# Performance work log

Hardware: AMD Instinct MI355X
Metric: run time of the kernel (lower is better)

Reference implementation:

```python
import jax, jax.numpy as jnp
import numpy as np

N = 262144   # total atoms (rows of x)
B = 512      # systems (segments)
E = 16       # experts
I = 256      # in_features
O_MOE = 128  # moe out channels (fraction_moe=0.5 of 256)
O_REG = 128  # regular Linear out channels


def setup_inputs() -> dict:
    key = jax.random.key(0)
    ks = jax.random.split(key, 6)
    k = 1.0 / np.sqrt(I)
    x = jax.random.normal(ks[0], (N, I), dtype=jnp.float32)
    coeff = jax.random.uniform(ks[1], (B, E), dtype=jnp.float32)
    routing_idxs = jnp.full((B,), N // B, dtype=jnp.int64)  # uniform segment lengths
    moe_weights = k * 2.0 * (jax.random.uniform(ks[2], (E, O_MOE, I), dtype=jnp.float32) - 0.5)
    moe_bias = k * 2.0 * (jax.random.uniform(ks[3], (O_MOE,), dtype=jnp.float32) - 0.5)
    lin_weight = k * 2.0 * (jax.random.uniform(ks[4], (O_REG, I), dtype=jnp.float32) - 0.5)
    lin_bias = k * 2.0 * (jax.random.uniform(ks[5], (O_REG,), dtype=jnp.float32) - 0.5)
    return {"x": x, "expert_mixing_coefficients": coeff, "routing_idxs": routing_idxs,
            "moe_weights": moe_weights, "moe_bias": moe_bias,
            "lin_weight": lin_weight, "lin_bias": lin_bias}


def reference(x, expert_mixing_coefficients, routing_idxs, moe_weights, moe_bias, lin_weight, lin_bias):
    b = expert_mixing_coefficients.shape[0]
    n, i = x.shape
    l = n // b  # uniform segment length (segment_mm with equal routing_idxs)
    # per-system mixed expert weights: [B, I, O_moe]
    w_mixed = jnp.einsum('eoi,be->bio', moe_weights, expert_mixing_coefficients)
    # grouped segment matmul: rows of segment b multiply w_mixed[b]
    moe_out = jnp.einsum('bli,bio->blo', x.reshape(b, l, i), w_mixed).reshape(n, -1) + moe_bias
    regular_out = x @ lin_weight.T + lin_bias
    return jnp.concatenate([moe_out, regular_out], axis=-1)
```

## Files before the change

kernel.cpp:

```cpp
#include <hip/hip_runtime.h>


#define NSEG   512
#define NEXP   16
#define KDIM   256
#define OMOE   128
#define OTOT   256
#define LSEG   512

typedef __attribute__((ext_vector_type(4))) float  f32x4;
typedef __attribute__((ext_vector_type(8))) short  bf16x8;
typedef __attribute__((ext_vector_type(4))) unsigned short u16x4;
typedef __attribute__((ext_vector_type(4))) unsigned int   u32x4;

__device__ __forceinline__ unsigned short bf16_rne(float v) {
  unsigned u = __builtin_bit_cast(unsigned, v);
  unsigned r = u + 0x7FFFu + ((u >> 16) & 1u);
  return (unsigned short)(r >> 16);
}
__device__ __forceinline__ void split2(float v, unsigned short& h, unsigned short& l) {
  h = bf16_rne(v);
  float hf = __builtin_bit_cast(float, ((unsigned)h) << 16);
  l = bf16_rne(v - hf);
}
__device__ __forceinline__ unsigned cvtpk(float a, float b) {
  unsigned r;
  asm("v_cvt_pk_bf16_f32 %0, %1, %2" : "=v"(r) : "v"(a), "v"(b));
  return r;
}
__device__ __forceinline__ void split8(f32x4 v0, f32x4 v1, bf16x8& h, bf16x8& l) {
  float a[8] = {v0[0], v0[1], v0[2], v0[3], v1[0], v1[1], v1[2], v1[3]};
  unsigned hw[4], lw[4];
  #pragma unroll
  for (int i = 0; i < 4; ++i) {
    unsigned hp = cvtpk(a[2 * i], a[2 * i + 1]);
    float hf0 = __builtin_bit_cast(float, hp << 16);
    float hf1 = __builtin_bit_cast(float, hp & 0xFFFF0000u);
    lw[i] = cvtpk(a[2 * i] - hf0, a[2 * i + 1] - hf1);
    hw[i] = hp;
  }
  u32x4 H = {hw[0], hw[1], hw[2], hw[3]};
  u32x4 L = {lw[0], lw[1], lw[2], lw[3]};
  h = __builtin_bit_cast(bf16x8, H);
  l = __builtin_bit_cast(bf16x8, L);
}


__global__ __launch_bounds__(256) void prep_moe_kernel(
    const float* __restrict__ moe_w, const float* __restrict__ coeff,
    unsigned short* __restrict__ wm) {
  __shared__ float wlds[NEXP][4][KDIM];
  const int t  = threadIdx.x;
  const int ot = blockIdx.x & 31;
  const int bc = blockIdx.x >> 5;
  const float* src = moe_w + (size_t)ot * 4 * KDIM;
  #pragma unroll
  for (int it = 0; it < 16; ++it) {
    int idx = it * 256 + t;
    int e = idx >> 8, rem = idx & 255;
    int o = rem >> 6, k4 = rem & 63;
    *(f32x4*)(&wlds[e][o][k4 * 4]) =
        *(const f32x4*)(src + (size_t)e * OMOE * KDIM + o * KDIM + k4 * 4);
  }
  __syncthreads();
  const int o = t >> 6, k4 = t & 63;
  const int og = ot * 4 + o;
  const int kt = k4 >> 3, ks = (k4 >> 1) & 3, jo = (k4 & 1) * 4;
  const int p  = og * 4 + (ks ^ ((og >> 1) & 3));
  const size_t woff = (size_t)kt * 8192 + p * 8 + jo;
  for (int bb = 0; bb < 32; ++bb) {
    const int b = bc * 32 + bb;
    const float* cf = coeff + (size_t)b * NEXP;
    f32x4 acc = (f32x4){0.f, 0.f, 0.f, 0.f};
    #pragma unroll
    for (int e = 0; e < NEXP; ++e) {
      const float c = cf[e];
      const f32x4 w = *(const f32x4*)(&wlds[e][o][k4 * 4]);
      #pragma unroll
      for (int j = 0; j < 4; ++j) acc[j] += c * w[j];
    }
    u16x4 hv, lv;
    #pragma unroll
    for (int j = 0; j < 4; ++j) {
      unsigned short h, l;
      split2(acc[j], h, l);
      hv[j] = h; lv[j] = l;
    }
    unsigned short* dst = wm + (size_t)b * 65536 + woff;
    *(u16x4*)(dst)        = hv;
    *(u16x4*)(dst + 4096) = lv;
  }
}

__global__ __launch_bounds__(256) void prep_lin_kernel(
    const float* __restrict__ lw, unsigned short* __restrict__ wl) {
  const int idx = blockIdx.x * 256 + threadIdx.x;
  const int o = idx >> 6, k4 = idx & 63;
  f32x4 v = *(const f32x4*)(lw + (size_t)idx * 4);
  const int kt = k4 >> 3, ks = (k4 >> 1) & 3, jo = (k4 & 1) * 4;
  const int p  = o * 4 + (ks ^ ((o >> 1) & 3));
  u16x4 hv, lv;
  #pragma unroll
  for (int j = 0; j < 4; ++j) {
    unsigned short h, l;
    split2(v[j], h, l);
    hv[j] = h; lv[j] = l;
  }
  unsigned short* dst = wl + (size_t)kt * 8192 + p * 8 + jo;
  *(u16x4*)(dst)        = hv;
  *(u16x4*)(dst + 4096) = lv;
}

#define GLOAD16(g, l) __builtin_amdgcn_global_load_lds(                      \
    (const __attribute__((address_space(1))) unsigned int*)(g),              \
    (__attribute__((address_space(3))) unsigned int*)(l), 16, 0, 0)

__global__ __launch_bounds__(512, 4) void gemm_kernel(
    const float* __restrict__ x,
    const unsigned short* __restrict__ wm, const unsigned short* __restrict__ wl,
    const float* __restrict__ moe_b, const float* __restrict__ lin_b,
    float* __restrict__ out) {
  __shared__ unsigned short lds[32768];
  const int t = threadIdx.x;
  const int wave = t >> 6, lane = t & 63;
  const int wrm = wave >> 1, wn = wave & 1;

  const int blk = blockIdx.x;
  const int wg = ((blk & 7) << 8) | (blk >> 3);
  const int b = wg >> 2, rt = wg & 3;
  const int row0 = b * LSEG + rt * 128;

  f32x4 acc[2][8] = {};

  const float* xbase = x + (size_t)(row0 + wrm * 32 + (lane & 15)) * KDIM + (lane >> 4) * 8;

  const int colb = wn * 128 + (lane & 15);
  const int ks = lane >> 4;
  const int boff0 = (colb * 4 + (ks ^ ((colb >> 1) & 3))) * 8;

  const unsigned short* wmb = wm + (size_t)b * 65536;

  auto stage_B = [&](int buf, int kt) {
    unsigned short* Bb = &lds[buf * 16384];
    const unsigned short* srcm = wmb + (size_t)kt * 8192;
    const unsigned short* srcl = wl  + (size_t)kt * 8192;
    #pragma unroll
    for (int part = 0; part < 2; ++part) {
      #pragma unroll
      for (int cc = 0; cc < 2; ++cc) {
        const int c = wave * 2 + cc;
        const unsigned short* src = (c < 8)
            ? (srcm + (size_t)part * 4096 + (c * 64 + lane) * 8)
            : (srcl + (size_t)part * 4096 + ((c - 8) * 64 + lane) * 8);
        GLOAD16(src, Bb + part * 8192 + c * 512);
      }
    }
  };

  bf16x8 ah[2], al[2];

  auto compute = [&](int buf) {
    const short* Bb = (const short*)&lds[buf * 16384];
    #pragma unroll
    for (int nt = 0; nt < 8; ++nt) {
      bf16x8 bh = *(const bf16x8*)(Bb + boff0 + nt * 512);
      bf16x8 bl = *(const bf16x8*)(Bb + 8192 + boff0 + nt * 512);
      #pragma unroll
      for (int mt = 0; mt < 2; ++mt) {
        acc[mt][nt] = __builtin_amdgcn_mfma_f32_16x16x32_bf16(ah[mt], bh, acc[mt][nt], 0, 0, 0);
        acc[mt][nt] = __builtin_amdgcn_mfma_f32_16x16x32_bf16(ah[mt], bl, acc[mt][nt], 0, 0, 0);
        acc[mt][nt] = __builtin_amdgcn_mfma_f32_16x16x32_bf16(al[mt], bh, acc[mt][nt], 0, 0, 0);
      }
    }
  };

  stage_B(0, 0);
  {
    const float* p0 = xbase;
    const float* p1 = xbase + 16 * KDIM;
    split8(*(const f32x4*)p0, *(const f32x4*)(p0 + 4), ah[0], al[0]);
    split8(*(const f32x4*)p1, *(const f32x4*)(p1 + 4), ah[1], al[1]);
  }
  __syncthreads();

  int buf = 0;
  for (int kt = 0; kt < 8; ++kt) {
    const bool pf = (kt < 7);
    f32x4 n0, n1, n2, n3;
    if (pf) {
      const float* p0 = xbase + (kt + 1) * 32;
      const float* p1 = p0 + 16 * KDIM;
      n0 = *(const f32x4*)p0; n1 = *(const f32x4*)(p0 + 4);
      n2 = *(const f32x4*)p1; n3 = *(const f32x4*)(p1 + 4);
      stage_B(buf ^ 1, kt + 1);
    }
    compute(buf);
    if (pf) {
      split8(n0, n1, ah[0], al[0]);
      split8(n2, n3, ah[1], al[1]);
    }
    __syncthreads();
    buf ^= 1;
  }

  #pragma unroll
  for (int nt = 0; nt < 8; ++nt) {
    const int col = wn * 128 + nt * 16 + (lane & 15);
    const float bias = (col < OMOE) ? moe_b[col] : lin_b[col - OMOE];
    #pragma unroll
    for (int mt = 0; mt < 2; ++mt) {
      const int rbase = row0 + wrm * 32 + mt * 16 + (lane >> 4) * 4;
      #pragma unroll
      for (int j = 0; j < 4; ++j)
        out[(size_t)(rbase + j) * OTOT + col] = acc[mt][nt][j] + bias;
    }
  }
}

extern "C" void kernel_launch(void* const* d_in, const int* in_sizes, int n_in,
                              void* d_out, int out_size, void* d_ws, size_t ws_size,
                              hipStream_t stream) {
  const float* x     = (const float*)d_in[0];
  const float* coeff = (const float*)d_in[1];
  const float* moe_w = (const float*)d_in[3];
  const float* moe_b = (const float*)d_in[4];
  const float* lin_w = (const float*)d_in[5];
  const float* lin_b = (const float*)d_in[6];
  float* out = (float*)d_out;

  unsigned short* wm = (unsigned short*)d_ws;
  unsigned short* wl = wm + (size_t)NSEG * 65536;

  prep_moe_kernel<<<dim3(512), dim3(256), 0, stream>>>(moe_w, coeff, wm);
  prep_lin_kernel<<<dim3(32), dim3(256), 0, stream>>>(lin_w, wl);
  gemm_kernel<<<dim3(2048), dim3(512), 0, stream>>>(x, wm, wl, moe_b, lin_b, out);
}
```

Baseline: 517.0 us.

## Split B staging into half-tile units with a deeper four-slot LDS ring

```diff
diff --git a/kernel.cpp b/kernel.cpp
--- a/kernel.cpp
+++ b/kernel.cpp
@@ -115,6 +115,8 @@
     (const __attribute__((address_space(1))) unsigned int*)(g),              \
     (__attribute__((address_space(3))) unsigned int*)(l), 16, 0, 0)
 
+#define MFMA(a, b, c) __builtin_amdgcn_mfma_f32_16x16x32_bf16((a), (b), (c), 0, 0, 0)
+
 __global__ __launch_bounds__(512, 4) void gemm_kernel(
     const float* __restrict__ x,
     const unsigned short* __restrict__ wm, const unsigned short* __restrict__ wl,
@@ -140,68 +142,84 @@
 
   const unsigned short* wmb = wm + (size_t)b * 65536;
 
-  auto stage_B = [&](int buf, int kt) {
-    unsigned short* Bb = &lds[buf * 16384];
-    const unsigned short* srcm = wmb + (size_t)kt * 8192;
-    const unsigned short* srcl = wl  + (size_t)kt * 8192;
-    #pragma unroll
-    for (int part = 0; part < 2; ++part) {
-      #pragma unroll
-      for (int cc = 0; cc < 2; ++cc) {
-        const int c = wave * 2 + cc;
-        const unsigned short* src = (c < 8)
-            ? (srcm + (size_t)part * 4096 + (c * 64 + lane) * 8)
-            : (srcl + (size_t)part * 4096 + ((c - 8) * 64 + lane) * 8);
-        GLOAD16(src, Bb + part * 8192 + c * 512);
-      }
+  auto stage_unit = [&](int u) {
+    const int kt = u >> 1, part = u & 1;
+    unsigned short* U = &lds[(u & 3) * 8192];
+    #pragma unroll
+    for (int cc = 0; cc < 2; ++cc) {
+      const int c = wave * 2 + cc;
+      const unsigned short* src = (c < 8)
+          ? (wmb + (size_t)kt * 8192 + part * 4096 + (c * 64 + lane) * 8)
+          : (wl  + (size_t)kt * 8192 + part * 4096 + ((c - 8) * 64 + lane) * 8);
+      GLOAD16(src, U + c * 512);
     }
   };
 
   bf16x8 ah[2], al[2];
 
-  auto compute = [&](int buf) {
-    const short* Bb = (const short*)&lds[buf * 16384];
+  auto compute_p0 = [&](int u) {
+    const short* U = (const short*)&lds[(u & 3) * 8192];
+    __builtin_amdgcn_s_setprio(1);
     #pragma unroll
     for (int nt = 0; nt < 8; ++nt) {
-      bf16x8 bh = *(const bf16x8*)(Bb + boff0 + nt * 512);
-      bf16x8 bl = *(const bf16x8*)(Bb + 8192 + boff0 + nt * 512);
-      #pragma unroll
-      for (int mt = 0; mt < 2; ++mt) {
-        acc[mt][nt] = __builtin_amdgcn_mfma_f32_16x16x32_bf16(ah[mt], bh, acc[mt][nt], 0, 0, 0);
-        acc[mt][nt] = __builtin_amdgcn_mfma_f32_16x16x32_bf16(ah[mt], bl, acc[mt][nt], 0, 0, 0);
-        acc[mt][nt] = __builtin_amdgcn_mfma_f32_16x16x32_bf16(al[mt], bh, acc[mt][nt], 0, 0, 0);
-      }
-    }
+      bf16x8 bh = *(const bf16x8*)(U + boff0 + nt * 512);
+      acc[0][nt] = MFMA(ah[0], bh, acc[0][nt]);
+      acc[1][nt] = MFMA(ah[1], bh, acc[1][nt]);
+      acc[0][nt] = MFMA(al[0], bh, acc[0][nt]);
+      acc[1][nt] = MFMA(al[1], bh, acc[1][nt]);
+    }
+    __builtin_amdgcn_s_setprio(0);
   };
-
-  stage_B(0, 0);
+  auto compute_p1 = [&](int u) {
+    const short* U = (const short*)&lds[(u & 3) * 8192];
+    __builtin_amdgcn_s_setprio(1);
+    #pragma unroll
+    for (int nt = 0; nt < 8; ++nt) {
+      bf16x8 bl = *(const bf16x8*)(U + boff0 + nt * 512);
+      acc[0][nt] = MFMA(ah[0], bl, acc[0][nt]);
+      acc[1][nt] = MFMA(ah[1], bl, acc[1][nt]);
+    }
+    __builtin_amdgcn_s_setprio(0);
+  };
+
+  stage_unit(0); stage_unit(1); stage_unit(2);
+  __builtin_amdgcn_sched_barrier(0);
   {
     const float* p0 = xbase;
     const float* p1 = xbase + 16 * KDIM;
     split8(*(const f32x4*)p0, *(const f32x4*)(p0 + 4), ah[0], al[0]);
     split8(*(const f32x4*)p1, *(const f32x4*)(p1 + 4), ah[1], al[1]);
   }
-  __syncthreads();
-
-  int buf = 0;
-  for (int kt = 0; kt < 8; ++kt) {
-    const bool pf = (kt < 7);
+  __builtin_amdgcn_s_barrier();
+  __builtin_amdgcn_sched_barrier(0);
+
+  for (int kt = 0; kt < 7; ++kt) {
+    const int u0 = kt * 2, u1 = u0 + 1;
+    stage_unit(u0 + 3);
+    __builtin_amdgcn_sched_barrier(0);
     f32x4 n0, n1, n2, n3;
-    if (pf) {
+    {
       const float* p0 = xbase + (kt + 1) * 32;
       const float* p1 = p0 + 16 * KDIM;
       n0 = *(const f32x4*)p0; n1 = *(const f32x4*)(p0 + 4);
       n2 = *(const f32x4*)p1; n3 = *(const f32x4*)(p1 + 4);
-      stage_B(buf ^ 1, kt + 1);
-    }
-    compute(buf);
-    if (pf) {
-      split8(n0, n1, ah[0], al[0]);
-      split8(n2, n3, ah[1], al[1]);
-    }
-    __syncthreads();
-    buf ^= 1;
-  }
+    }
+    compute_p0(u0);
+    __builtin_amdgcn_s_barrier();
+    __builtin_amdgcn_sched_barrier(0);
+    if (kt < 6) stage_unit(u1 + 3);
+    __builtin_amdgcn_sched_barrier(0);
+    compute_p1(u1);
+    split8(n0, n1, ah[0], al[0]);
+    split8(n2, n3, ah[1], al[1]);
+    asm volatile("s_waitcnt vmcnt(2)" ::: "memory");
+    __builtin_amdgcn_s_barrier();
+    __builtin_amdgcn_sched_barrier(0);
+  }
+
+  compute_p0(14);
+  __syncthreads();
+  compute_p1(15);
 
   #pragma unroll
   for (int nt = 0; nt < 8; ++nt) {
```

New measurement: 514.8 us. Within noise of the previous version (-0.4%).

## Switch GEMM to 32x32x16 MFMA with matching weight layout and staging

Applied to the files above, without the earlier changes.

```diff
diff --git a/kernel.cpp b/kernel.cpp
--- a/kernel.cpp
+++ b/kernel.cpp
@@ -8,10 +8,11 @@
 #define OTOT   256
 #define LSEG   512
 
-typedef __attribute__((ext_vector_type(4))) float  f32x4;
-typedef __attribute__((ext_vector_type(8))) short  bf16x8;
-typedef __attribute__((ext_vector_type(4))) unsigned short u16x4;
-typedef __attribute__((ext_vector_type(4))) unsigned int   u32x4;
+typedef __attribute__((ext_vector_type(4)))  float  f32x4;
+typedef __attribute__((ext_vector_type(16))) float  f32x16;
+typedef __attribute__((ext_vector_type(8)))  short  bf16x8;
+typedef __attribute__((ext_vector_type(4)))  unsigned short u16x4;
+typedef __attribute__((ext_vector_type(4)))  unsigned int   u32x4;
 
 __device__ __forceinline__ unsigned short bf16_rne(float v) {
   unsigned u = __builtin_bit_cast(unsigned, v);
@@ -65,9 +66,8 @@
   __syncthreads();
   const int o = t >> 6, k4 = t & 63;
   const int og = ot * 4 + o;
-  const int kt = k4 >> 3, ks = (k4 >> 1) & 3, jo = (k4 & 1) * 4;
-  const int p  = og * 4 + (ks ^ ((og >> 1) & 3));
-  const size_t woff = (size_t)kt * 8192 + p * 8 + jo;
+  const int kt = k4 >> 3, s = (k4 >> 2) & 1, kc = (k4 >> 1) & 1, jo = (k4 & 1) * 4;
+  const size_t woff = (size_t)kt * 8192 + ((s * 2 + kc) * 128 + og) * 8 + jo;
   for (int bb = 0; bb < 32; ++bb) {
     const int b = bc * 32 + bb;
     const float* cf = coeff + (size_t)b * NEXP;
@@ -97,8 +97,7 @@
   const int idx = blockIdx.x * 256 + threadIdx.x;
   const int o = idx >> 6, k4 = idx & 63;
   f32x4 v = *(const f32x4*)(lw + (size_t)idx * 4);
-  const int kt = k4 >> 3, ks = (k4 >> 1) & 3, jo = (k4 & 1) * 4;
-  const int p  = o * 4 + (ks ^ ((o >> 1) & 3));
+  const int kt = k4 >> 3, s = (k4 >> 2) & 1, kc = (k4 >> 1) & 1, jo = (k4 & 1) * 4;
   u16x4 hv, lv;
   #pragma unroll
   for (int j = 0; j < 4; ++j) {
@@ -106,7 +105,7 @@
     split2(v[j], h, l);
     hv[j] = h; lv[j] = l;
   }
-  unsigned short* dst = wl + (size_t)kt * 8192 + p * 8 + jo;
+  unsigned short* dst = wl + (size_t)kt * 8192 + ((s * 2 + kc) * 128 + o) * 8 + jo;
   *(u16x4*)(dst)        = hv;
   *(u16x4*)(dst + 4096) = lv;
 }
@@ -114,6 +113,8 @@
 #define GLOAD16(g, l) __builtin_amdgcn_global_load_lds(                      \
     (const __attribute__((address_space(1))) unsigned int*)(g),              \
     (__attribute__((address_space(3))) unsigned int*)(l), 16, 0, 0)
+
+#define MFMA32(a, b, c) __builtin_amdgcn_mfma_f32_32x32x16_bf16((a), (b), (c), 0, 0, 0)
 
 __global__ __launch_bounds__(512, 4) void gemm_kernel(
     const float* __restrict__ x,
@@ -124,36 +125,30 @@
   const int t = threadIdx.x;
   const int wave = t >> 6, lane = t & 63;
   const int wrm = wave >> 1, wn = wave & 1;
+  const int lanec = lane & 31, kc = lane >> 5;
 
   const int blk = blockIdx.x;
   const int wg = ((blk & 7) << 8) | (blk >> 3);
   const int b = wg >> 2, rt = wg & 3;
   const int row0 = b * LSEG + rt * 128;
 
-  f32x4 acc[2][8] = {};
-
-  const float* xbase = x + (size_t)(row0 + wrm * 32 + (lane & 15)) * KDIM + (lane >> 4) * 8;
-
-  const int colb = wn * 128 + (lane & 15);
-  const int ks = lane >> 4;
-  const int boff0 = (colb * 4 + (ks ^ ((colb >> 1) & 3))) * 8;
+  f32x16 acc[4] = {};
+
+  const float* xbase = x + (size_t)(row0 + wrm * 32 + lanec) * KDIM + kc * 8;
+
+  const int base_rd = (kc * 256 + wn * 128 + lanec) * 8;
 
   const unsigned short* wmb = wm + (size_t)b * 65536;
 
-  auto stage_B = [&](int buf, int kt) {
-    unsigned short* Bb = &lds[buf * 16384];
-    const unsigned short* srcm = wmb + (size_t)kt * 8192;
-    const unsigned short* srcl = wl  + (size_t)kt * 8192;
-    #pragma unroll
-    for (int part = 0; part < 2; ++part) {
-      #pragma unroll
-      for (int cc = 0; cc < 2; ++cc) {
-        const int c = wave * 2 + cc;
-        const unsigned short* src = (c < 8)
-            ? (srcm + (size_t)part * 4096 + (c * 64 + lane) * 8)
-            : (srcl + (size_t)part * 4096 + ((c - 8) * 64 + lane) * 8);
-        GLOAD16(src, Bb + part * 8192 + c * 512);
-      }
+  auto stage = [&](int buf, int kt) {
+    unsigned short* D = &lds[buf * 16384 + wave * 2048];
+    const unsigned short* sm = wmb + (size_t)kt * 8192 + wave * 1024;
+    const unsigned short* sl = wl  + (size_t)kt * 8192 + wave * 1024;
+    #pragma unroll
+    for (int cc = 0; cc < 4; ++cc) {
+      const unsigned short* src = (cc < 2) ? (sm + (cc * 64 + lane) * 8)
+                                           : (sl + ((cc - 2) * 64 + lane) * 8);
+      GLOAD16(src, D + cc * 512);
     }
   };
 
@@ -162,22 +157,27 @@
   auto compute = [&](int buf) {
     const short* Bb = (const short*)&lds[buf * 16384];
     #pragma unroll
-    for (int nt = 0; nt < 8; ++nt) {
-      bf16x8 bh = *(const bf16x8*)(Bb + boff0 + nt * 512);
-      bf16x8 bl = *(const bf16x8*)(Bb + 8192 + boff0 + nt * 512);
-      #pragma unroll
-      for (int mt = 0; mt < 2; ++mt) {
-        acc[mt][nt] = __builtin_amdgcn_mfma_f32_16x16x32_bf16(ah[mt], bh, acc[mt][nt], 0, 0, 0);
-        acc[mt][nt] = __builtin_amdgcn_mfma_f32_16x16x32_bf16(ah[mt], bl, acc[mt][nt], 0, 0, 0);
-        acc[mt][nt] = __builtin_amdgcn_mfma_f32_16x16x32_bf16(al[mt], bh, acc[mt][nt], 0, 0, 0);
-      }
+    for (int s = 0; s < 2; ++s) {
+      bf16x8 bf[4];
+      #pragma unroll
+      for (int nt = 0; nt < 4; ++nt)
+        bf[nt] = *(const bf16x8*)(Bb + base_rd + s * 4096 + nt * 256);
+      #pragma unroll
+      for (int nt = 0; nt < 4; ++nt) acc[nt] = MFMA32(ah[s], bf[nt], acc[nt]);
+      #pragma unroll
+      for (int nt = 0; nt < 4; ++nt) acc[nt] = MFMA32(al[s], bf[nt], acc[nt]);
+      #pragma unroll
+      for (int nt = 0; nt < 4; ++nt)
+        bf[nt] = *(const bf16x8*)(Bb + 8192 + base_rd + s * 4096 + nt * 256);
+      #pragma unroll
+      for (int nt = 0; nt < 4; ++nt) acc[nt] = MFMA32(ah[s], bf[nt], acc[nt]);
     }
   };
 
-  stage_B(0, 0);
+  stage(0, 0);
   {
     const float* p0 = xbase;
-    const float* p1 = xbase + 16 * KDIM;
+    const float* p1 = xbase + 16;
     split8(*(const f32x4*)p0, *(const f32x4*)(p0 + 4), ah[0], al[0]);
     split8(*(const f32x4*)p1, *(const f32x4*)(p1 + 4), ah[1], al[1]);
   }
@@ -189,10 +189,10 @@
     f32x4 n0, n1, n2, n3;
     if (pf) {
       const float* p0 = xbase + (kt + 1) * 32;
-      const float* p1 = p0 + 16 * KDIM;
+      const float* p1 = p0 + 16;
       n0 = *(const f32x4*)p0; n1 = *(const f32x4*)(p0 + 4);
       n2 = *(const f32x4*)p1; n3 = *(const f32x4*)(p1 + 4);
-      stage_B(buf ^ 1, kt + 1);
+      stage(buf ^ 1, kt + 1);
     }
     compute(buf);
     if (pf) {
@@ -204,15 +204,14 @@
   }
 
   #pragma unroll
-  for (int nt = 0; nt < 8; ++nt) {
-    const int col = wn * 128 + nt * 16 + (lane & 15);
+  for (int nt = 0; nt < 4; ++nt) {
+    const int col = wn * 128 + nt * 32 + lanec;
     const float bias = (col < OMOE) ? moe_b[col] : lin_b[col - OMOE];
-    #pragma unroll
-    for (int mt = 0; mt < 2; ++mt) {
-      const int rbase = row0 + wrm * 32 + mt * 16 + (lane >> 4) * 4;
-      #pragma unroll
-      for (int j = 0; j < 4; ++j)
-        out[(size_t)(rbase + j) * OTOT + col] = acc[mt][nt][j] + bias;
+    const int rbase = row0 + wrm * 32 + 4 * kc;
+    #pragma unroll
+    for (int reg = 0; reg < 16; ++reg) {
+      const int row = rbase + (reg & 3) + 8 * (reg >> 2);
+      out[(size_t)row * OTOT + col] = acc[nt][reg] + bias;
     }
   }
 }
```

Result: no change. 517.5 us (+0.1%).
